# Kernel optimization log

Measured on AMD Instinct MI355X. Metric: run time of the kernel, lower is better.

Reference implementation:

```python
import jax, jax.numpy as jnp
import numpy as np

B, T, H, L, V = 16, 512, 512, 2, 32000

def setup_inputs() -> dict:
    key = jax.random.key(0)
    k1, k2, k3, k4 = jax.random.split(key, 4)
    tokens = jax.random.randint(k1, (B, T), 0, V)
    embed = jax.random.normal(k2, (V, H), dtype=jnp.float32) * 0.02
    W = jax.random.normal(k3, (L, 2 * H, 4 * H), dtype=jnp.float32) * (1.0 / np.sqrt(2 * H))
    b = jnp.zeros((L, 4 * H), dtype=jnp.float32)
    Wout = jax.random.normal(k4, (H, V), dtype=jnp.float32) * (1.0 / np.sqrt(H))
    bout = jnp.zeros((V,), dtype=jnp.float32)
    return {"tokens": tokens, "embed": embed, "W": W, "b": b, "Wout": Wout, "bout": bout}

def _run_layer(h_seq, Wl, bl):
    # h_seq: [T, B, H]
    hid = Wl.shape[1] // 4
    def step(carry, x_t):
        c, h = carry
        gates = jnp.concatenate([x_t, h], axis=-1) @ Wl + bl  # [B, 4H]
        i, f, g, o = jnp.split(gates, 4, axis=-1)
        i = jax.nn.sigmoid(i)
        f = jax.nn.sigmoid(f)
        g = jnp.tanh(g)
        o = jax.nn.sigmoid(o)
        new_c = f * c + i * g
        new_h = o * jnp.tanh(new_c)
        return (new_c, new_h), new_h
    Bsz = h_seq.shape[1]
    init = (jnp.zeros((Bsz, hid), h_seq.dtype), jnp.zeros((Bsz, hid), h_seq.dtype))
    _, out = jax.lax.scan(step, init, h_seq)
    return out  # [T, B, H]

def reference(tokens, embed, W, b, Wout, bout):
    h = embed[tokens]                     # [B, T, H]
    h = jnp.transpose(h, (1, 0, 2))       # [T, B, H] for scan
    for l in range(W.shape[0]):
        h = _run_layer(h, W[l], b[l])
    h = jnp.transpose(h, (1, 0, 2))       # [B, T, H]
    logits = h @ Wout + bout              # [B, T, V]
    return logits
```

## Files before the change

### kernel.cpp

```cpp
#include <hip/hip_runtime.h>
#include <stdint.h>

#define Tn 512
#define Hn 512
#define Vn 32000
#define KIN 1024
#define G4 2048
#define NBLK 256
#define PHASES 513
#define PSTR 40
#define XSTR 1032
#define SLOT_STRIDE 2048

typedef __attribute__((ext_vector_type(8))) short short8;
typedef __attribute__((ext_vector_type(4))) float f32x4;
typedef __attribute__((ext_vector_type(4))) int i32x4;
typedef __attribute__((ext_vector_type(4))) unsigned u32x4;

__device__ __forceinline__ unsigned short f2bf(float v) {
  unsigned int x = __float_as_uint(v);
  return (unsigned short)((x + 0x7fffu + ((x >> 16) & 1u)) >> 16);
}
__device__ __forceinline__ float bf2f(unsigned short u) {
  return __uint_as_float(((unsigned int)u) << 16);
}
__device__ __forceinline__ unsigned pollld(const unsigned* p) {
  return __hip_atomic_load(p, __ATOMIC_RELAXED, __HIP_MEMORY_SCOPE_AGENT);
}
__device__ __forceinline__ void flagst(unsigned* p, unsigned v) {
  __hip_atomic_store(p, v, __ATOMIC_RELAXED, __HIP_MEMORY_SCOPE_AGENT);
}

__device__ __forceinline__ void stage_unpack_sc1(const unsigned* src,
                                                 unsigned short* Xh,
                                                 unsigned short* Xl, int off) {
  u32x4 a, b, c, d;
  asm volatile(
      "global_load_dwordx4 %0, %4, off sc1\n\t"
      "global_load_dwordx4 %1, %5, off sc1\n\t"
      "global_load_dwordx4 %2, %6, off sc1\n\t"
      "global_load_dwordx4 %3, %7, off sc1\n\t"
      "s_waitcnt vmcnt(0)"
      : "=&v"(a), "=&v"(b), "=&v"(c), "=&v"(d)
      : "v"(src), "v"(src + 4), "v"(src + 8), "v"(src + 12)
      : "memory");
  unsigned u[16];
#pragma unroll
  for (int i = 0; i < 4; ++i) {
    u[i] = a[i]; u[4 + i] = b[i]; u[8 + i] = c[i]; u[12 + i] = d[i];
  }
  unsigned hw[8], lw[8];
#pragma unroll
  for (int j = 0; j < 8; ++j) {
    const unsigned e0 = u[2 * j], e1 = u[2 * j + 1];
    hw[j] = (e0 >> 16) | (e1 & 0xffff0000u);
    lw[j] = (e0 & 0xffffu) | (e1 << 16);
  }
  *(u32x4*)&Xh[off]     = *(const u32x4*)&hw[0];
  *(u32x4*)&Xh[off + 8] = *(const u32x4*)&hw[4];
  *(u32x4*)&Xl[off]     = *(const u32x4*)&lw[0];
  *(u32x4*)&Xl[off + 8] = *(const u32x4*)&lw[4];
}

__device__ __forceinline__ void stage_f32(const float* src, unsigned short* Xh,
                                          unsigned short* Xl, int off) {
  const f32x4 v0 = *(const f32x4*)src;
  const f32x4 v1 = *(const f32x4*)(src + 4);
  const f32x4 v2 = *(const f32x4*)(src + 8);
  const f32x4 v3 = *(const f32x4*)(src + 12);
  unsigned short h16[16], l16[16];
#pragma unroll
  for (int i = 0; i < 4; ++i) {
    float x;
    x = v0[i]; h16[i]      = f2bf(x); l16[i]      = f2bf(x - bf2f(h16[i]));
    x = v1[i]; h16[4 + i]  = f2bf(x); l16[4 + i]  = f2bf(x - bf2f(h16[4 + i]));
    x = v2[i]; h16[8 + i]  = f2bf(x); l16[8 + i]  = f2bf(x - bf2f(h16[8 + i]));
    x = v3[i]; h16[12 + i] = f2bf(x); l16[12 + i] = f2bf(x - bf2f(h16[12 + i]));
  }
  *(u32x4*)&Xh[off]     = *(const u32x4*)&h16[0];
  *(u32x4*)&Xh[off + 8] = *(const u32x4*)&h16[8];
  *(u32x4*)&Xl[off]     = *(const u32x4*)&l16[0];
  *(u32x4*)&Xl[off + 8] = *(const u32x4*)&l16[8];
}

__global__ __launch_bounds__(256) void wout_convert(const float* __restrict__ Wout,
                                                    unsigned short* __restrict__ BhT,
                                                    unsigned short* __restrict__ BlT) {
  __shared__ float ts[64][65];
  const int n0 = blockIdx.x * 64;
  const int k0 = blockIdx.y * 64;
  const int tid = threadIdx.x;
  {
    const int c = tid & 63, rq = tid >> 6;
#pragma unroll
    for (int i = 0; i < 16; ++i) {
      const int k = rq * 16 + i;
      ts[k][c] = Wout[(size_t)(k0 + k) * Vn + (n0 + c)];
    }
  }
  __syncthreads();
  {
    const int nl = tid >> 2;
    const int ks = (tid & 3) * 16;
    unsigned short hb[16], lb[16];
#pragma unroll
    for (int i = 0; i < 16; ++i) {
      const float v = ts[ks + i][nl];
      const unsigned short h = f2bf(v);
      hb[i] = h;
      lb[i] = f2bf(v - bf2f(h));
    }
    const size_t base = (size_t)(n0 + nl) * Hn + (k0 + ks);
    *(i32x4*)&BhT[base]     = *(const i32x4*)&hb[0];
    *(i32x4*)&BhT[base + 8] = *(const i32x4*)&hb[8];
    *(i32x4*)&BlT[base]     = *(const i32x4*)&lb[0];
    *(i32x4*)&BlT[base + 8] = *(const i32x4*)&lb[8];
  }
}

__global__ __launch_bounds__(512) void lstm_scan(
    const int* __restrict__ tokens, const float* __restrict__ embed,
    const float* __restrict__ Wg, const float* __restrict__ bg,
    unsigned* __restrict__ hex1, unsigned* __restrict__ hex2,
    unsigned short* __restrict__ Ah, unsigned short* __restrict__ Al,
    unsigned* __restrict__ arr) {

  extern __shared__ char smembytes[];
  unsigned short* Wh  = (unsigned short*)smembytes;
  unsigned short* Wlo = Wh + 16 * XSTR;
  unsigned short* Xh  = Wlo + 16 * XSTR;
  unsigned short* Xl  = Xh + 16 * XSTR;
  float* red   = (float*)(Xl + 16 * XSTR);
  float* gates = red + 8 * 272;
  float* cst   = gates + 256;

  const int tid = threadIdx.x;
  const int bid = blockIdx.x;
  const int layer = bid >> 7;
  const int u0 = (bid & 127) * 4;

  for (int idx = tid; idx < 16 * KIN; idx += 512) {
    const int k = idx >> 4;
    const int c = idx & 15;
    const int col = ((c >> 2) << 9) + u0 + (c & 3);
    const float wv = Wg[(size_t)layer * KIN * G4 + (size_t)k * G4 + col];
    const unsigned short h = f2bf(wv);
    Wh[c * XSTR + k] = h;
    Wlo[c * XSTR + k] = f2bf(wv - bf2f(h));
  }
  if (tid < 64) cst[tid] = 0.f;

  float bb0 = 0.f, bb1 = 0.f, bb2 = 0.f, bb3 = 0.f;
  if (tid < 64) {
    const int j = tid & 3;
    bb0 = bg[layer * G4 + 0 * 512 + u0 + j];
    bb1 = bg[layer * G4 + 1 * 512 + u0 + j];
    bb2 = bg[layer * G4 + 2 * 512 + u0 + j];
    bb3 = bg[layer * G4 + 3 * 512 + u0 + j];
  }

  const int lane = tid & 63;
  const int w = tid >> 6;
  const int srow = tid >> 5;
  const int kseg = (tid & 31) * 16;
  const int m = lane & 15;
  const int g8 = (lane >> 4) * 8;
  unsigned* myslot = (unsigned*)((char*)arr + (size_t)bid * SLOT_STRIDE);
  const unsigned* pollslot =
      (const unsigned*)((const char*)arr + (size_t)(tid & 255) * SLOT_STRIDE);

  __syncthreads();

  if (layer == 0) {
    const int tok = tokens[srow * Tn + 0];
    stage_f32(embed + (size_t)tok * Hn + kseg, Xh, Xl, srow * XSTR + kseg);
  }

  for (int ph = 0; ph < PHASES; ++ph) {
    const unsigned target = (unsigned)(ph + 1);
    const bool act = (layer == 0) ? (ph < Tn) : (ph >= 1);

    if (act) {
      const unsigned* h1p = hex1 + ((ph - 1) & 1) * 8192 + srow * 512 + kseg;
      if (layer == 0) {
        stage_unpack_sc1(h1p, Xh, Xl, srow * XSTR + 512 + kseg);
      } else {
        stage_unpack_sc1(h1p, Xh, Xl, srow * XSTR + kseg);
        stage_unpack_sc1(hex2 + (ph & 1) * 8192 + srow * 512 + kseg,
                         Xh, Xl, srow * XSTR + 512 + kseg);
      }
    }
    __syncthreads();

    if (act) {
      f32x4 acc = {0.f, 0.f, 0.f, 0.f};
#pragma unroll
      for (int it = 0; it < 4; ++it) {
        const int kb = w * 128 + it * 32 + g8;
        const short8 ahf = *(const short8*)&Xh[m * XSTR + kb];
        const short8 alf = *(const short8*)&Xl[m * XSTR + kb];
        const short8 bhf = *(const short8*)&Wh[m * XSTR + kb];
        const short8 blf = *(const short8*)&Wlo[m * XSTR + kb];
        acc = __builtin_amdgcn_mfma_f32_16x16x32_bf16(ahf, bhf, acc, 0, 0, 0);
        acc = __builtin_amdgcn_mfma_f32_16x16x32_bf16(ahf, blf, acc, 0, 0, 0);
        acc = __builtin_amdgcn_mfma_f32_16x16x32_bf16(alf, bhf, acc, 0, 0, 0);
      }
      const int r0 = (lane >> 4) * 4;
#pragma unroll
      for (int r = 0; r < 4; ++r)
        red[w * 272 + (r0 + r) * 17 + m] = acc[r];
    }
    __syncthreads();

    if (act && tid < 256) {
      const int b = tid >> 4, c = tid & 15;
      float s = 0.f;
#pragma unroll
      for (int ww = 0; ww < 8; ++ww) s += red[ww * 272 + b * 17 + c];
      gates[tid] = s;
    }
    __syncthreads();

    if (act && tid < 64) {
      const int b = tid >> 2, j = tid & 3;
      const float gi = gates[b * 16 + j] + bb0;
      const float gf = gates[b * 16 + 4 + j] + bb1;
      const float gg = gates[b * 16 + 8 + j] + bb2;
      const float go = gates[b * 16 + 12 + j] + bb3;
      const float si = 1.f / (1.f + expf(-gi));
      const float sf = 1.f / (1.f + expf(-gf));
      const float tg = tanhf(gg);
      const float so = 1.f / (1.f + expf(-go));
      const float cn = sf * cst[tid] + si * tg;
      cst[tid] = cn;
      const float hn = so * tanhf(cn);
      const unsigned short hh = f2bf(hn);
      const unsigned short hl = f2bf(hn - bf2f(hh));
      const unsigned pk = ((unsigned)hh << 16) | (unsigned)hl;
      unsigned* hdst = (layer == 0)
          ? hex1 + (ph & 1) * 8192 + b * 512 + (u0 + j)
          : hex2 + ((ph - 1) & 1) * 8192 + b * 512 + (u0 + j);
      flagst(hdst, pk);
      if (layer == 1) {
        const size_t r = (size_t)(ph - 1) * 16 + b;
        Ah[r * Hn + u0 + j] = hh;
        Al[r * Hn + u0 + j] = hl;
      }
    }
    __syncthreads();

    if (tid == 0) flagst(myslot, target);

    if (layer == 0 && (ph + 1) < Tn) {
      const int tok = tokens[srow * Tn + (ph + 1)];
      stage_f32(embed + (size_t)tok * Hn + kseg, Xh, Xl, srow * XSTR + kseg);
    }
    if (tid < 256) {
      while (pollld(pollslot) < target) __builtin_amdgcn_s_sleep(2);
    }
    __syncthreads();
  }
}

__global__ __launch_bounds__(256) void proj_gemm(
    const unsigned short* __restrict__ Ah_, const unsigned short* __restrict__ Al_,
    const unsigned short* __restrict__ Bh_, const unsigned short* __restrict__ Bl_,
    const float* __restrict__ bout, float* __restrict__ out) {
  __shared__ unsigned short sAh[128 * PSTR], sAl[128 * PSTR], sBh[128 * PSTR], sBl[128 * PSTR];
  const int tid = threadIdx.x;
  const int n0 = blockIdx.x * 128;
  const int m0 = blockIdx.y * 128;
  const int lane = tid & 63, w = tid >> 6;
  const int wm = (w & 1) * 64, wn = (w >> 1) * 64;

  f32x4 acc[4][4];
#pragma unroll
  for (int i = 0; i < 4; ++i)
#pragma unroll
    for (int j = 0; j < 4; ++j) acc[i][j] = (f32x4){0.f, 0.f, 0.f, 0.f};

  for (int kt = 0; kt < 16; ++kt) {
    const int k0 = kt * 32;
    __syncthreads();
#pragma unroll
    for (int i = 0; i < 8; ++i) {
      const int chunk = ((i & 1) << 8) + tid;
      const int mrow = chunk >> 2;
      const int kc = chunk & 3;
      const int tsel = i >> 1;
      const unsigned short* gsrc =
          (tsel == 0) ? Ah_ + (size_t)(m0 + mrow) * Hn + k0 + kc * 8 :
          (tsel == 1) ? Al_ + (size_t)(m0 + mrow) * Hn + k0 + kc * 8 :
          (tsel == 2) ? Bh_ + (size_t)(n0 + mrow) * Hn + k0 + kc * 8 :
                        Bl_ + (size_t)(n0 + mrow) * Hn + k0 + kc * 8;
      unsigned short* ldst = (tsel == 0) ? sAh : (tsel == 1) ? sAl : (tsel == 2) ? sBh : sBl;
      *(i32x4*)&ldst[mrow * PSTR + kc * 8] = *(const i32x4*)gsrc;
    }
    __syncthreads();

    short8 fah[4], fal[4], fbh[4], fbl[4];
    const int rlo = lane & 15, kg = (lane >> 4) * 8;
#pragma unroll
    for (int f = 0; f < 4; ++f) {
      fah[f] = *(const short8*)&sAh[(wm + f * 16 + rlo) * PSTR + kg];
      fal[f] = *(const short8*)&sAl[(wm + f * 16 + rlo) * PSTR + kg];
      fbh[f] = *(const short8*)&sBh[(wn + f * 16 + rlo) * PSTR + kg];
      fbl[f] = *(const short8*)&sBl[(wn + f * 16 + rlo) * PSTR + kg];
    }
#pragma unroll
    for (int i = 0; i < 4; ++i)
#pragma unroll
      for (int j = 0; j < 4; ++j) {
        acc[i][j] = __builtin_amdgcn_mfma_f32_16x16x32_bf16(fah[i], fbh[j], acc[i][j], 0, 0, 0);
        acc[i][j] = __builtin_amdgcn_mfma_f32_16x16x32_bf16(fah[i], fbl[j], acc[i][j], 0, 0, 0);
        acc[i][j] = __builtin_amdgcn_mfma_f32_16x16x32_bf16(fal[i], fbh[j], acc[i][j], 0, 0, 0);
      }
  }

#pragma unroll
  for (int j = 0; j < 4; ++j) {
    const int n = n0 + wn + j * 16 + (lane & 15);
    const float bv = bout[n];
#pragma unroll
    for (int i = 0; i < 4; ++i) {
#pragma unroll
      for (int r = 0; r < 4; ++r) {
        const int m = m0 + wm + i * 16 + ((lane >> 4) * 4) + r;
        out[(size_t)(m & 15) * ((size_t)Tn * Vn) + (size_t)(m >> 4) * Vn + n] =
            acc[i][j][r] + bv;
      }
    }
  }
}

extern "C" void kernel_launch(void* const* d_in, const int* in_sizes, int n_in,
                              void* d_out, int out_size, void* d_ws, size_t ws_size,
                              hipStream_t stream) {
  const int*   tokens = (const int*)d_in[0];
  const float* embed  = (const float*)d_in[1];
  const float* W      = (const float*)d_in[2];
  const float* bias   = (const float*)d_in[3];
  const float* Wout   = (const float*)d_in[4];
  const float* bout   = (const float*)d_in[5];
  float* out = (float*)d_out;

  char* ws = (char*)d_ws;
  unsigned* arr  = (unsigned*)ws;
  unsigned* hex1 = (unsigned*)(ws + 524288);
  unsigned* hex2 = (unsigned*)(ws + 524288 + 65536);
  unsigned short* Ah  = (unsigned short*)(ws + 655360);
  unsigned short* Al  = Ah + (size_t)8192 * 512;
  unsigned short* BhT = Al + (size_t)8192 * 512;
  unsigned short* BlT = BhT + (size_t)32000 * 512;

  hipMemsetAsync(d_ws, 0, 655360, stream);

  wout_convert<<<dim3(500, 8), 256, 0, stream>>>(Wout, BhT, BlT);

  const size_t ldsbytes = (size_t)(4 * 16 * XSTR) * 2 +
                          (size_t)(8 * 272 + 256 + 64) * 4;
  (void)hipFuncSetAttribute((const void*)lstm_scan,
                            hipFuncAttributeMaxDynamicSharedMemorySize, (int)ldsbytes);
  lstm_scan<<<NBLK, 512, ldsbytes, stream>>>(tokens, embed, W, bias,
                                             hex1, hex2, Ah, Al, arr);

  proj_gemm<<<dim3(250, 64), 256, 0, stream>>>(Ah, Al, BhT, BlT, bout, out);
}
```

Before: 3.312 ms.

## Compact grid barrier flags and shorten per-step sync path in LSTM scan

```diff
diff --git a/kernel.cpp b/kernel.cpp
--- a/kernel.cpp
+++ b/kernel.cpp
@@ -10,7 +10,6 @@
 #define PHASES 513
 #define PSTR 40
 #define XSTR 1032
-#define SLOT_STRIDE 2048
 
 typedef __attribute__((ext_vector_type(8))) short short8;
 typedef __attribute__((ext_vector_type(4))) float f32x4;
@@ -24,17 +23,13 @@
 __device__ __forceinline__ float bf2f(unsigned short u) {
   return __uint_as_float(((unsigned int)u) << 16);
 }
-__device__ __forceinline__ unsigned pollld(const unsigned* p) {
-  return __hip_atomic_load(p, __ATOMIC_RELAXED, __HIP_MEMORY_SCOPE_AGENT);
-}
 __device__ __forceinline__ void flagst(unsigned* p, unsigned v) {
   __hip_atomic_store(p, v, __ATOMIC_RELAXED, __HIP_MEMORY_SCOPE_AGENT);
 }
 
-__device__ __forceinline__ void stage_unpack_sc1(const unsigned* src,
-                                                 unsigned short* Xh,
-                                                 unsigned short* Xl, int off) {
-  u32x4 a, b, c, d;
+__device__ __forceinline__ void ld4x4_sc1(const unsigned* p0, const unsigned* p1,
+                                          const unsigned* p2, const unsigned* p3,
+                                          u32x4& a, u32x4& b, u32x4& c, u32x4& d) {
   asm volatile(
       "global_load_dwordx4 %0, %4, off sc1\n\t"
       "global_load_dwordx4 %1, %5, off sc1\n\t"
@@ -42,45 +37,56 @@
       "global_load_dwordx4 %3, %7, off sc1\n\t"
       "s_waitcnt vmcnt(0)"
       : "=&v"(a), "=&v"(b), "=&v"(c), "=&v"(d)
-      : "v"(src), "v"(src + 4), "v"(src + 8), "v"(src + 12)
+      : "v"(p0), "v"(p1), "v"(p2), "v"(p3)
       : "memory");
-  unsigned u[16];
+}
+__device__ __forceinline__ void ld8x4_sc1(
+    const unsigned* p0, const unsigned* p1, const unsigned* p2, const unsigned* p3,
+    const unsigned* p4, const unsigned* p5, const unsigned* p6, const unsigned* p7,
+    u32x4& a, u32x4& b, u32x4& c, u32x4& d,
+    u32x4& e, u32x4& f, u32x4& g, u32x4& h) {
+  asm volatile(
+      "global_load_dwordx4 %0, %8, off sc1\n\t"
+      "global_load_dwordx4 %1, %9, off sc1\n\t"
+      "global_load_dwordx4 %2, %10, off sc1\n\t"
+      "global_load_dwordx4 %3, %11, off sc1\n\t"
+      "global_load_dwordx4 %4, %12, off sc1\n\t"
+      "global_load_dwordx4 %5, %13, off sc1\n\t"
+      "global_load_dwordx4 %6, %14, off sc1\n\t"
+      "global_load_dwordx4 %7, %15, off sc1\n\t"
+      "s_waitcnt vmcnt(0)"
+      : "=&v"(a), "=&v"(b), "=&v"(c), "=&v"(d),
+        "=&v"(e), "=&v"(f), "=&v"(g), "=&v"(h)
+      : "v"(p0), "v"(p1), "v"(p2), "v"(p3),
+        "v"(p4), "v"(p5), "v"(p6), "v"(p7)
+      : "memory");
+}
+
+__device__ __forceinline__ void unpack8(const u32x4& a, const u32x4& b,
+                                        unsigned short* XhDst, unsigned short* XlDst) {
+  unsigned hw[4], lw[4];
+  hw[0] = (a[0] >> 16) | (a[1] & 0xffff0000u);
+  lw[0] = (a[0] & 0xffffu) | (a[1] << 16);
+  hw[1] = (a[2] >> 16) | (a[3] & 0xffff0000u);
+  lw[1] = (a[2] & 0xffffu) | (a[3] << 16);
+  hw[2] = (b[0] >> 16) | (b[1] & 0xffff0000u);
+  lw[2] = (b[0] & 0xffffu) | (b[1] << 16);
+  hw[3] = (b[2] >> 16) | (b[3] & 0xffff0000u);
+  lw[3] = (b[2] & 0xffffu) | (b[3] << 16);
+  *(u32x4*)XhDst = *(const u32x4*)hw;
+  *(u32x4*)XlDst = *(const u32x4*)lw;
+}
+
+__device__ __forceinline__ void cvt8(const f32x4& v0, const f32x4& v1,
+                                     unsigned short* XhDst, unsigned short* XlDst) {
+  unsigned short h8[8], l8[8];
 #pragma unroll
   for (int i = 0; i < 4; ++i) {
-    u[i] = a[i]; u[4 + i] = b[i]; u[8 + i] = c[i]; u[12 + i] = d[i];
-  }
-  unsigned hw[8], lw[8];
-#pragma unroll
-  for (int j = 0; j < 8; ++j) {
-    const unsigned e0 = u[2 * j], e1 = u[2 * j + 1];
-    hw[j] = (e0 >> 16) | (e1 & 0xffff0000u);
-    lw[j] = (e0 & 0xffffu) | (e1 << 16);
-  }
-  *(u32x4*)&Xh[off]     = *(const u32x4*)&hw[0];
-  *(u32x4*)&Xh[off + 8] = *(const u32x4*)&hw[4];
-  *(u32x4*)&Xl[off]     = *(const u32x4*)&lw[0];
-  *(u32x4*)&Xl[off + 8] = *(const u32x4*)&lw[4];
-}
-
-__device__ __forceinline__ void stage_f32(const float* src, unsigned short* Xh,
-                                          unsigned short* Xl, int off) {
-  const f32x4 v0 = *(const f32x4*)src;
-  const f32x4 v1 = *(const f32x4*)(src + 4);
-  const f32x4 v2 = *(const f32x4*)(src + 8);
-  const f32x4 v3 = *(const f32x4*)(src + 12);
-  unsigned short h16[16], l16[16];
-#pragma unroll
-  for (int i = 0; i < 4; ++i) {
-    float x;
-    x = v0[i]; h16[i]      = f2bf(x); l16[i]      = f2bf(x - bf2f(h16[i]));
-    x = v1[i]; h16[4 + i]  = f2bf(x); l16[4 + i]  = f2bf(x - bf2f(h16[4 + i]));
-    x = v2[i]; h16[8 + i]  = f2bf(x); l16[8 + i]  = f2bf(x - bf2f(h16[8 + i]));
-    x = v3[i]; h16[12 + i] = f2bf(x); l16[12 + i] = f2bf(x - bf2f(h16[12 + i]));
-  }
-  *(u32x4*)&Xh[off]     = *(const u32x4*)&h16[0];
-  *(u32x4*)&Xh[off + 8] = *(const u32x4*)&h16[8];
-  *(u32x4*)&Xl[off]     = *(const u32x4*)&l16[0];
-  *(u32x4*)&Xl[off + 8] = *(const u32x4*)&l16[8];
+    h8[i]     = f2bf(v0[i]); l8[i]     = f2bf(v0[i] - bf2f(h8[i]));
+    h8[4 + i] = f2bf(v1[i]); l8[4 + i] = f2bf(v1[i] - bf2f(h8[4 + i]));
+  }
+  *(u32x4*)XhDst = *(const u32x4*)h8;
+  *(u32x4*)XlDst = *(const u32x4*)l8;
 }
 
 __global__ __launch_bounds__(256) void wout_convert(const float* __restrict__ Wout,
@@ -130,9 +136,7 @@
   unsigned short* Wlo = Wh + 16 * XSTR;
   unsigned short* Xh  = Wlo + 16 * XSTR;
   unsigned short* Xl  = Xh + 16 * XSTR;
-  float* red   = (float*)(Xl + 16 * XSTR);
-  float* gates = red + 8 * 272;
-  float* cst   = gates + 256;
+  float* red = (float*)(Xl + 16 * XSTR);
 
   const int tid = threadIdx.x;
   const int bid = blockIdx.x;
@@ -148,9 +152,8 @@
     Wh[c * XSTR + k] = h;
     Wlo[c * XSTR + k] = f2bf(wv - bf2f(h));
   }
-  if (tid < 64) cst[tid] = 0.f;
-
-  float bb0 = 0.f, bb1 = 0.f, bb2 = 0.f, bb3 = 0.f;
+
+  float bb0 = 0.f, bb1 = 0.f, bb2 = 0.f, bb3 = 0.f, c_state = 0.f;
   if (tid < 64) {
     const int j = tid & 3;
     bb0 = bg[layer * G4 + 0 * 512 + u0 + j];
@@ -161,19 +164,24 @@
 
   const int lane = tid & 63;
   const int w = tid >> 6;
-  const int srow = tid >> 5;
-  const int kseg = (tid & 31) * 16;
   const int m = lane & 15;
   const int g8 = (lane >> 4) * 8;
-  unsigned* myslot = (unsigned*)((char*)arr + (size_t)bid * SLOT_STRIDE);
-  const unsigned* pollslot =
-      (const unsigned*)((const char*)arr + (size_t)(tid & 255) * SLOT_STRIDE);
+
+  const int gA = tid, gB = tid + 512;
+  const int rowA = gA >> 6, slotA = gA & 63;
+  const int rowB = gB >> 6, slotB = gB & 63;
+  const int offA = rowA * XSTR + slotA * 8;
+  const int offB = rowB * XSTR + slotB * 8;
 
   __syncthreads();
 
   if (layer == 0) {
-    const int tok = tokens[srow * Tn + 0];
-    stage_f32(embed + (size_t)tok * Hn + kseg, Xh, Xl, srow * XSTR + kseg);
+    const int tokA = tokens[rowA * Tn + 0];
+    const int tokB = tokens[rowB * Tn + 0];
+    const float* sA = embed + (size_t)tokA * Hn + slotA * 8;
+    const float* sB = embed + (size_t)tokB * Hn + slotB * 8;
+    cvt8(*(const f32x4*)sA, *(const f32x4*)(sA + 4), &Xh[offA], &Xl[offA]);
+    cvt8(*(const f32x4*)sB, *(const f32x4*)(sB + 4), &Xh[offB], &Xl[offB]);
   }
 
   for (int ph = 0; ph < PHASES; ++ph) {
@@ -181,13 +189,24 @@
     const bool act = (layer == 0) ? (ph < Tn) : (ph >= 1);
 
     if (act) {
-      const unsigned* h1p = hex1 + ((ph - 1) & 1) * 8192 + srow * 512 + kseg;
       if (layer == 0) {
-        stage_unpack_sc1(h1p, Xh, Xl, srow * XSTR + 512 + kseg);
+        const unsigned* hb = hex1 + ((ph - 1) & 1) * 8192;
+        u32x4 a0, a1, b0, b1;
+        ld4x4_sc1(hb + gA * 8, hb + gA * 8 + 4, hb + gB * 8, hb + gB * 8 + 4,
+                  a0, a1, b0, b1);
+        unpack8(a0, a1, &Xh[offA + 512], &Xl[offA + 512]);
+        unpack8(b0, b1, &Xh[offB + 512], &Xl[offB + 512]);
       } else {
-        stage_unpack_sc1(h1p, Xh, Xl, srow * XSTR + kseg);
-        stage_unpack_sc1(hex2 + (ph & 1) * 8192 + srow * 512 + kseg,
-                         Xh, Xl, srow * XSTR + 512 + kseg);
+        const unsigned* xb = hex1 + ((ph - 1) & 1) * 8192;
+        const unsigned* hb = hex2 + (ph & 1) * 8192;
+        u32x4 x0, x1, x2, x3, h0, h1v, h2v, h3;
+        ld8x4_sc1(xb + gA * 8, xb + gA * 8 + 4, xb + gB * 8, xb + gB * 8 + 4,
+                  hb + gA * 8, hb + gA * 8 + 4, hb + gB * 8, hb + gB * 8 + 4,
+                  x0, x1, x2, x3, h0, h1v, h2v, h3);
+        unpack8(x0, x1, &Xh[offA], &Xl[offA]);
+        unpack8(x2, x3, &Xh[offB], &Xl[offB]);
+        unpack8(h0, h1v, &Xh[offA + 512], &Xl[offA + 512]);
+        unpack8(h2v, h3, &Xh[offB + 512], &Xl[offB + 512]);
       }
     }
     __syncthreads();
@@ -212,28 +231,24 @@
     }
     __syncthreads();
 
-    if (act && tid < 256) {
-      const int b = tid >> 4, c = tid & 15;
-      float s = 0.f;
-#pragma unroll
-      for (int ww = 0; ww < 8; ++ww) s += red[ww * 272 + b * 17 + c];
-      gates[tid] = s;
-    }
-    __syncthreads();
-
     if (act && tid < 64) {
       const int b = tid >> 2, j = tid & 3;
-      const float gi = gates[b * 16 + j] + bb0;
-      const float gf = gates[b * 16 + 4 + j] + bb1;
-      const float gg = gates[b * 16 + 8 + j] + bb2;
-      const float go = gates[b * 16 + 12 + j] + bb3;
-      const float si = 1.f / (1.f + expf(-gi));
-      const float sf = 1.f / (1.f + expf(-gf));
-      const float tg = tanhf(gg);
-      const float so = 1.f / (1.f + expf(-go));
-      const float cn = sf * cst[tid] + si * tg;
-      cst[tid] = cn;
-      const float hn = so * tanhf(cn);
+      float g4[4] = {bb0, bb1, bb2, bb3};
+#pragma unroll
+      for (int g = 0; g < 4; ++g) {
+        const int c = g * 4 + j;
+#pragma unroll
+        for (int ww = 0; ww < 8; ++ww) g4[g] += red[ww * 272 + b * 17 + c];
+      }
+      const float si = 1.f / (1.f + __expf(-g4[0]));
+      const float sf = 1.f / (1.f + __expf(-g4[1]));
+      const float e2g = __expf(2.f * g4[2]);
+      const float tg = 1.f - 2.f / (e2g + 1.f);
+      const float so = 1.f / (1.f + __expf(-g4[3]));
+      const float cn = sf * c_state + si * tg;
+      c_state = cn;
+      const float e2c = __expf(2.f * cn);
+      const float hn = so * (1.f - 2.f / (e2c + 1.f));
       const unsigned short hh = f2bf(hn);
       const unsigned short hl = f2bf(hn - bf2f(hh));
       const unsigned pk = ((unsigned)hh << 16) | (unsigned)hl;
@@ -247,16 +262,32 @@
         Al[r * Hn + u0 + j] = hl;
       }
     }
-    __syncthreads();
-
-    if (tid == 0) flagst(myslot, target);
+    if (tid < 64) {
+      asm volatile("s_waitcnt vmcnt(0)" ::: "memory");
+      if (tid == 0) flagst(arr + bid, target);
+    }
 
     if (layer == 0 && (ph + 1) < Tn) {
-      const int tok = tokens[srow * Tn + (ph + 1)];
-      stage_f32(embed + (size_t)tok * Hn + kseg, Xh, Xl, srow * XSTR + kseg);
-    }
-    if (tid < 256) {
-      while (pollld(pollslot) < target) __builtin_amdgcn_s_sleep(2);
+      const int t1 = ph + 1;
+      const int tokA = tokens[rowA * Tn + t1];
+      const int tokB = tokens[rowB * Tn + t1];
+      const float* sA = embed + (size_t)tokA * Hn + slotA * 8;
+      const float* sB = embed + (size_t)tokB * Hn + slotB * 8;
+      cvt8(*(const f32x4*)sA, *(const f32x4*)(sA + 4), &Xh[offA], &Xl[offA]);
+      cvt8(*(const f32x4*)sB, *(const f32x4*)(sB + 4), &Xh[offB], &Xl[offB]);
+    }
+
+    if (tid < 64) {
+      const unsigned* pp = arr + lane * 4;
+      for (;;) {
+        u32x4 v;
+        asm volatile("global_load_dwordx4 %0, %1, off sc1\n\ts_waitcnt vmcnt(0)"
+                     : "=&v"(v) : "v"(pp) : "memory");
+        const bool ok = v[0] >= target && v[1] >= target &&
+                        v[2] >= target && v[3] >= target;
+        if (__all(ok)) break;
+        __builtin_amdgcn_s_sleep(2);
+      }
     }
     __syncthreads();
   }
@@ -346,19 +377,18 @@
 
   char* ws = (char*)d_ws;
   unsigned* arr  = (unsigned*)ws;
-  unsigned* hex1 = (unsigned*)(ws + 524288);
-  unsigned* hex2 = (unsigned*)(ws + 524288 + 65536);
-  unsigned short* Ah  = (unsigned short*)(ws + 655360);
+  unsigned* hex1 = (unsigned*)(ws + 4096);
+  unsigned* hex2 = (unsigned*)(ws + 4096 + 65536);
+  unsigned short* Ah  = (unsigned short*)(ws + 135168);
   unsigned short* Al  = Ah + (size_t)8192 * 512;
   unsigned short* BhT = Al + (size_t)8192 * 512;
   unsigned short* BlT = BhT + (size_t)32000 * 512;
 
-  hipMemsetAsync(d_ws, 0, 655360, stream);
+  hipMemsetAsync(d_ws, 0, 135168, stream);
 
   wout_convert<<<dim3(500, 8), 256, 0, stream>>>(Wout, BhT, BlT);
 
-  const size_t ldsbytes = (size_t)(4 * 16 * XSTR) * 2 +
-                          (size_t)(8 * 272 + 256 + 64) * 4;
+  const size_t ldsbytes = (size_t)(4 * 16 * XSTR) * 2 + (size_t)(8 * 272) * 4;
   (void)hipFuncSetAttribute((const void*)lstm_scan,
                             hipFuncAttributeMaxDynamicSharedMemorySize, (int)ldsbytes);
   lstm_scan<<<NBLK, 512, ldsbytes, stream>>>(tokens, embed, W, bias,
```

Measured after the change: 4.214 ms. +27.3%, slower.
